# Kernel optimization log

Hardware: AMD Instinct MI355X
Metric: run time of the kernel (lower is better)

## Reference

```python
import jax, jax.numpy as jnp
import numpy as np

B, S, E = 4, 2048, 1024
H = 16
HD = E // H  # head_dim = 64


def setup_inputs() -> dict:
    key = jax.random.key(0)
    ks = jax.random.split(key, 12)
    sc = 0.02
    return {
        "q_encodings": jax.random.normal(ks[0], (B, S, E), jnp.float32),
        "k_encodings": jax.random.normal(ks[1], (B, S, E), jnp.float32),
        "v_encodings": jax.random.normal(ks[2], (B, S, E), jnp.float32),
        # per-head q/k/v linear weights [H, HD, HD] and biases [H, HD]
        "Wq": jax.random.normal(ks[3], (H, HD, HD), jnp.float32) * sc,
        "bq": jax.random.normal(ks[4], (H, HD), jnp.float32) * sc,
        "Wk": jax.random.normal(ks[5], (H, HD, HD), jnp.float32) * sc,
        "bk": jax.random.normal(ks[6], (H, HD), jnp.float32) * sc,
        "Wv": jax.random.normal(ks[7], (H, HD, HD), jnp.float32) * sc,
        "bv": jax.random.normal(ks[8], (H, HD), jnp.float32) * sc,
        # output projection [E, E] + bias [E]
        "Wp": jax.random.normal(ks[9], (E, E), jnp.float32) * sc,
        "bp": jax.random.normal(ks[10], (E,), jnp.float32) * sc,
        "mask": 1,
    }


def reference(q_encodings, k_encodings, v_encodings, Wq, bq, Wk, bk, Wv, bv, Wp, bp, mask):
    b, s, e = q_encodings.shape
    h, hd, _ = Wq.shape
    split = lambda x: x.reshape(b, s, h, hd)  # per-head slices of n_embd
    # batched per-head linear projections (original loops over heads)
    Q = jnp.einsum('bshd,hde->bshe', split(q_encodings), Wq) + bq
    K = jnp.einsum('bshd,hde->bshe', split(k_encodings), Wk) + bk
    V = jnp.einsum('bshd,hde->bshe', split(v_encodings), Wv) + bv
    # scaled dot-product scores [B,H,S,S]; scale uses head_dim (Attention.n_embd)
    scores = jnp.einsum('bqhd,bkhd->bhqk', Q, K) / jnp.sqrt(jnp.float32(hd))
    if mask:  # static Python flag, matches torch `if mask:`
        causal = jnp.tril(jnp.ones((s, s), jnp.float32))
        scores = scores + jnp.where(causal == 0, jnp.float32(-jnp.inf), jnp.float32(0.0))
    attn = jax.nn.softmax(scores, axis=-1)
    ctx = jnp.einsum('bhqk,bkhd->bqhd', attn, V).reshape(b, s, e)
    return ctx @ Wp + bp
```

## Files before the change

kernel.cpp:

```cpp
#include <hip/hip_runtime.h>
#include <hip/hip_bf16.h>
#include <math.h>

typedef __bf16 bf16;
typedef __bf16 bf16x8 __attribute__((ext_vector_type(8)));
typedef float f32x4 __attribute__((ext_vector_type(4)));
typedef unsigned int u32x2 __attribute__((ext_vector_type(2)));

constexpr int B = 4, S = 2048, E = 1024, H = 16, HD = 64;

constexpr float QSCALE = 0.125f * 1.44269504088896340736f;
constexpr float DTHR = 11.5f;

static __device__ __forceinline__ float exp2_fast(float x) {
#if __has_builtin(__builtin_amdgcn_exp2f)
    return __builtin_amdgcn_exp2f(x);
#else
    float r; asm("v_exp_f32 %0, %1" : "=v"(r) : "v"(x)); return r;
#endif
}

static __device__ __forceinline__ unsigned pk_bf16(float a, float b) {
    union { bf16 h[2]; unsigned u; } r;
    r.h[0] = (bf16)a; r.h[1] = (bf16)b;
    return r.u;
}

__global__ __launch_bounds__(256) void prep_weights(
    const float* __restrict__ Wq, const float* __restrict__ Wk,
    const float* __restrict__ Wv, const float* __restrict__ Wp,
    bf16* __restrict__ Wt, bf16* __restrict__ Wpt)
{
    __shared__ float t[64][65];
    const int tid = threadIdx.x;
    const int x = blockIdx.x, y = blockIdx.y;
    if (y < 3) {
        const int h = x, p = y;
        const float* W = (p == 0) ? Wq : (p == 1) ? Wk : Wv;
        const float scale = (p == 0) ? QSCALE : 1.0f;
        #pragma unroll
        for (int i = 0; i < 16; ++i) {
            int idx = tid + i * 256;
            int d = idx >> 6, e = idx & 63;
            t[d][e] = W[(size_t)h * 4096 + d * 64 + e];
        }
        __syncthreads();
        bf16* dst = Wt + ((size_t)p * H + h) * 4096;
        #pragma unroll
        for (int i = 0; i < 16; ++i) {
            int idx = tid + i * 256;
            int e = idx >> 6, d = idx & 63;
            dst[e * 64 + d] = (bf16)(t[d][e] * scale);
        }
    } else {
        const int k0 = (y - 3) * 64, n0 = x * 64;
        #pragma unroll
        for (int i = 0; i < 16; ++i) {
            int idx = tid + i * 256;
            int r = idx >> 6, c = idx & 63;
            t[r][c] = Wp[(size_t)(k0 + r) * E + n0 + c];
        }
        __syncthreads();
        #pragma unroll
        for (int i = 0; i < 16; ++i) {
            int idx = tid + i * 256;
            int r = idx >> 6, c = idx & 63;
            Wpt[(size_t)(n0 + r) * E + k0 + c] = (bf16)t[c][r];
        }
    }
}

__global__ __launch_bounds__(256) void qkv_proj(
    const float* __restrict__ xq, const float* __restrict__ xk, const float* __restrict__ xv,
    const bf16* __restrict__ Wt,
    const float* __restrict__ bq, const float* __restrict__ bk, const float* __restrict__ bv,
    bf16* __restrict__ Qb, bf16* __restrict__ Kb, bf16* __restrict__ Vt)
{
    const int b = blockIdx.z, h = blockIdx.y, s0 = blockIdx.x * 128;
    const int tid = threadIdx.x;
    const int w = tid >> 6, l = tid & 63;
    const int l16 = l & 15, lg = l >> 4;
    const size_t bh = (size_t)b * H + h;

    __shared__ __align__(16) bf16 xs[128][64];
    __shared__ __align__(16) bf16 Wl[64][64];
    __shared__ __align__(16) bf16 ts[10240];

    for (int p = 0; p < 3; ++p) {
        const float* x    = (p == 0) ? xq : (p == 1) ? xk : xv;
        const float* bias = (p == 0) ? bq : (p == 1) ? bk : bv;
        const float  bsc  = (p == 0) ? QSCALE : 1.0f;

        __syncthreads();
        #pragma unroll
        for (int i = 0; i < 4; ++i) {
            int idx = tid + i * 256;
            int r = idx >> 3, g = idx & 7;
            const float* src = &x[((size_t)b * S + s0 + r) * E + h * 64 + g * 8];
            float4 f0 = *(const float4*)src;
            float4 f1 = *(const float4*)(src + 4);
            union { bf16 h8[8]; uint4 u; } pk;
            pk.h8[0] = (bf16)f0.x; pk.h8[1] = (bf16)f0.y;
            pk.h8[2] = (bf16)f0.z; pk.h8[3] = (bf16)f0.w;
            pk.h8[4] = (bf16)f1.x; pk.h8[5] = (bf16)f1.y;
            pk.h8[6] = (bf16)f1.z; pk.h8[7] = (bf16)f1.w;
            *(uint4*)&xs[r][(g ^ (r & 7)) * 8] = pk.u;
        }
        const bf16* wsrc = Wt + ((size_t)p * H + h) * 4096;
        #pragma unroll
        for (int i = 0; i < 2; ++i) {
            int idx = tid + i * 256;
            int e = idx >> 3, g = idx & 7;
            *(uint4*)&Wl[e][(g ^ (e & 7)) * 8] = *(const uint4*)(wsrc + e * 64 + g * 8);
        }
        __syncthreads();

        if (p < 2) {
            float bcol[4];
            #pragma unroll
            for (int ei = 0; ei < 4; ++ei)
                bcol[ei] = bias[h * 64 + ei * 16 + l16] * bsc;
            #pragma unroll
            for (int st = 0; st < 2; ++st) {
                const int srow = w * 32 + st * 16 + l16;
                bf16x8 a0 = *(const bf16x8*)&xs[srow][((lg    ) ^ (srow & 7)) * 8];
                bf16x8 a1 = *(const bf16x8*)&xs[srow][((4 + lg) ^ (srow & 7)) * 8];
                #pragma unroll
                for (int ei = 0; ei < 4; ++ei) {
                    const int erow = ei * 16 + l16;
                    bf16x8 b0 = *(const bf16x8*)&Wl[erow][((lg    ) ^ (erow & 7)) * 8];
                    bf16x8 b1 = *(const bf16x8*)&Wl[erow][((4 + lg) ^ (erow & 7)) * 8];
                    f32x4 acc = {0.f, 0.f, 0.f, 0.f};
                    acc = __builtin_amdgcn_mfma_f32_16x16x32_bf16(a0, b0, acc, 0, 0, 0);
                    acc = __builtin_amdgcn_mfma_f32_16x16x32_bf16(a1, b1, acc, 0, 0, 0);
                    #pragma unroll
                    for (int r = 0; r < 4; ++r)
                        ts[(w * 32 + st * 16 + 4 * lg + r) * 80 + ei * 16 + l16] =
                            (bf16)(acc[r] + bcol[ei]);
                }
            }
            __syncthreads();
            bf16* out = (p == 0) ? Qb : Kb;
            #pragma unroll
            for (int i = 0; i < 4; ++i) {
                int idx = tid + i * 256;
                int r = idx >> 3, g = idx & 7;
                uint4 v = *(const uint4*)&ts[r * 80 + g * 8];
                *(uint4*)(out + (bh * S + s0 + r) * 64 + g * 8) = v;
            }
        } else {
            float brow[4];
            #pragma unroll
            for (int r = 0; r < 4; ++r)
                brow[r] = bias[h * 64 + w * 16 + 4 * lg + r];
            const int erow = w * 16 + l16;
            bf16x8 a0 = *(const bf16x8*)&Wl[erow][((lg    ) ^ (erow & 7)) * 8];
            bf16x8 a1 = *(const bf16x8*)&Wl[erow][((4 + lg) ^ (erow & 7)) * 8];
            #pragma unroll
            for (int st = 0; st < 8; ++st) {
                const int srow = st * 16 + l16;
                bf16x8 b0 = *(const bf16x8*)&xs[srow][((lg    ) ^ (srow & 7)) * 8];
                bf16x8 b1 = *(const bf16x8*)&xs[srow][((4 + lg) ^ (srow & 7)) * 8];
                f32x4 acc = {0.f, 0.f, 0.f, 0.f};
                acc = __builtin_amdgcn_mfma_f32_16x16x32_bf16(a0, b0, acc, 0, 0, 0);
                acc = __builtin_amdgcn_mfma_f32_16x16x32_bf16(a1, b1, acc, 0, 0, 0);
                #pragma unroll
                for (int r = 0; r < 4; ++r)
                    ts[(w * 16 + 4 * lg + r) * 136 + st * 16 + l16] =
                        (bf16)(acc[r] + brow[r]);
            }
            __syncthreads();
            #pragma unroll
            for (int i = 0; i < 4; ++i) {
                int idx = tid + i * 256;
                int r = idx >> 4, g = idx & 15;
                uint4 v = *(const uint4*)&ts[r * 136 + g * 8];
                *(uint4*)(Vt + (bh * 64 + r) * S + s0 + g * 8) = v;
            }
        }
    }
}

__global__ __launch_bounds__(512) void attn(
    const bf16* __restrict__ Qb, const bf16* __restrict__ Kb,
    const bf16* __restrict__ Vt, bf16* __restrict__ ctx)
{
    const int pair = blockIdx.x;
    const int bh   = blockIdx.y;
    const int b = bh >> 4, h = bh & 15;
    const int tid = threadIdx.x;
    const int w = tid >> 6;
    const int l = tid & 63;
    const int l16 = l & 15, lg = l >> 4;

    __shared__ __align__(16) bf16 Kl[2][64][64];
    __shared__ __align__(16) bf16 Vl[2][64][64];
    __shared__ __align__(16) bf16 Pl[8][16][72];

    const bf16* Qp = Qb + (size_t)bh * S * 64;
    const bf16* Kp = Kb + (size_t)bh * S * 64;
    const bf16* Vp = Vt + (size_t)bh * 64 * S;

    const int str = tid >> 3;
    const int stc = tid & 7;
    const int sws = (stc ^ (str & 7)) * 8;

    int foff0[4], foff1[4];
    #pragma unroll
    for (int s = 0; s < 4; ++s) {
        foff0[s] = (16 * s + l16) * 64 + ((lg    ) ^ (l16 & 7)) * 8;
        foff1[s] = (16 * s + l16) * 64 + ((4 + lg) ^ (l16 & 7)) * 8;
    }
    bf16* Plw = &Pl[w][0][0];
    const int pwr = l16 * 72 + 4 * lg;
    const int prd = l16 * 72 + 8 * lg;

    const bf16 one_ = (bf16)1.0f;
    const bf16x8 ones = {one_, one_, one_, one_, one_, one_, one_, one_};

    #pragma unroll 1
    for (int half = 0; half < 2; ++half) {
        const int qt   = half ? (15 - pair) : pair;
        const int qw0  = qt * 128 + w * 16;
        const int qabs = qw0 + l16;
        const int nt   = 2 * qt + 2;

        bf16x8 qf0 = *(const bf16x8*)(Qp + (size_t)qabs * 64 + lg * 8);
        bf16x8 qf1 = *(const bf16x8*)(Qp + (size_t)qabs * 64 + 32 + lg * 8);

        f32x4 o[4] = {};
        float m_run = -1e30f, l_run = 0.f;

        {
            uint4 kreg = *(const uint4*)(Kp + (size_t)str * 64 + stc * 8);
            uint4 vreg = *(const uint4*)(Vp + (size_t)str * S + stc * 8);
            *(uint4*)&Kl[0][str][sws] = kreg;
            *(uint4*)&Vl[0][str][sws] = vreg;
        }
        int cur = 0;
        for (int t = 0; t < nt; ++t) {
            __syncthreads();
            const bool pfv = (t + 1 < nt);
            uint4 kreg, vreg;
            if (pfv) {
                const int kv1 = (t + 1) * 64;
                kreg = *(const uint4*)(Kp + (size_t)(kv1 + str) * 64 + stc * 8);
                vreg = *(const uint4*)(Vp + (size_t)str * S + kv1 + stc * 8);
            }
            const int kv0 = t * 64;
            if (kv0 < qw0 + 16) {
                const bf16* Kbase = &Kl[cur][0][0];
                const bf16* Vbase = &Vl[cur][0][0];

                float p[16];
                __builtin_amdgcn_s_setprio(1);
                #pragma unroll
                for (int s = 0; s < 4; ++s) {
                    f32x4 sc = {0.f, 0.f, 0.f, 0.f};
                    bf16x8 ka = *(const bf16x8*)(Kbase + foff0[s]);
                    bf16x8 kb = *(const bf16x8*)(Kbase + foff1[s]);
                    sc = __builtin_amdgcn_mfma_f32_16x16x32_bf16(ka, qf0, sc, 0, 0, 0);
                    sc = __builtin_amdgcn_mfma_f32_16x16x32_bf16(kb, qf1, sc, 0, 0, 0);
                    p[4 * s + 0] = sc[0]; p[4 * s + 1] = sc[1];
                    p[4 * s + 2] = sc[2]; p[4 * s + 3] = sc[3];
                }
                __builtin_amdgcn_s_setprio(0);

                if (kv0 + 63 > qw0) {
                    #pragma unroll
                    for (int i = 0; i < 16; ++i) {
                        const int kvloc = 16 * (i >> 2) + 4 * lg + (i & 3);
                        if (kv0 + kvloc > qabs) p[i] = -1e30f;
                    }
                }

                float mx = p[0];
                #pragma unroll
                for (int i = 1; i < 16; ++i) mx = fmaxf(mx, p[i]);
                mx = fmaxf(mx, __shfl_xor(mx, 16));
                mx = fmaxf(mx, __shfl_xor(mx, 32));
                if (!__all(mx <= m_run + DTHR)) {
                    const float m_new = fmaxf(m_run, mx);
                    const float corr = exp2_fast(m_run - m_new);
                    l_run *= corr;
                    #pragma unroll
                    for (int ds = 0; ds < 4; ++ds) {
                        o[ds][0] *= corr; o[ds][1] *= corr;
                        o[ds][2] *= corr; o[ds][3] *= corr;
                    }
                    m_run = m_new;
                }
                #pragma unroll
                for (int i = 0; i < 16; ++i) p[i] = exp2_fast(p[i] - m_run);

                #pragma unroll
                for (int s = 0; s < 4; ++s) {
                    u32x2 pw;
                    pw[0] = pk_bf16(p[4 * s + 0], p[4 * s + 1]);
                    pw[1] = pk_bf16(p[4 * s + 2], p[4 * s + 3]);
                    *(u32x2*)(Plw + pwr + 16 * s) = pw;
                }
                asm volatile("s_waitcnt lgkmcnt(0)" ::: "memory");
                bf16x8 pf0 = *(const bf16x8*)(Plw + prd);
                bf16x8 pf1 = *(const bf16x8*)(Plw + prd + 32);

                __builtin_amdgcn_s_setprio(1);
                f32x4 o5 = {0.f, 0.f, 0.f, 0.f};
                o5 = __builtin_amdgcn_mfma_f32_16x16x32_bf16(ones, pf0, o5, 0, 0, 0);
                o5 = __builtin_amdgcn_mfma_f32_16x16x32_bf16(ones, pf1, o5, 0, 0, 0);
                #pragma unroll
                for (int ds = 0; ds < 4; ++ds) {
                    bf16x8 v0 = *(const bf16x8*)(Vbase + foff0[ds]);
                    bf16x8 v1 = *(const bf16x8*)(Vbase + foff1[ds]);
                    o[ds] = __builtin_amdgcn_mfma_f32_16x16x32_bf16(v0, pf0, o[ds], 0, 0, 0);
                    o[ds] = __builtin_amdgcn_mfma_f32_16x16x32_bf16(v1, pf1, o[ds], 0, 0, 0);
                }
                __builtin_amdgcn_s_setprio(0);
                l_run += o5[0];
            }
            if (pfv) {
                *(uint4*)&Kl[cur ^ 1][str][sws] = kreg;
                *(uint4*)&Vl[cur ^ 1][str][sws] = vreg;
            }
            cur ^= 1;
        }

        const float il = 1.0f / l_run;
        bf16* crow = ctx + ((size_t)b * S + qabs) * E + h * 64;
        #pragma unroll
        for (int ds = 0; ds < 4; ++ds) {
            u32x2 pw;
            pw[0] = pk_bf16(o[ds][0] * il, o[ds][1] * il);
            pw[1] = pk_bf16(o[ds][2] * il, o[ds][3] * il);
            *(u32x2*)(crow + 16 * ds + 4 * lg) = pw;
        }
    }
}

__global__ __launch_bounds__(256) void out_gemm(
    const bf16* __restrict__ A, const bf16* __restrict__ Bt,
    const float* __restrict__ bp, float* __restrict__ C)
{
    const int n0 = blockIdx.x * 128, m0 = blockIdx.y * 128;
    const int tid = threadIdx.x;
    const int w = tid >> 6, l = tid & 63;
    const int l16 = l & 15, lg = l >> 4;
    const int wm = w >> 1, wn = w & 1;

    __shared__ __align__(16) bf16 Al[128][64];
    __shared__ __align__(16) bf16 Bl[128][64];

    f32x4 acc[4][4] = {};

    for (int k0 = 0; k0 < E; k0 += 64) {
        __syncthreads();
        #pragma unroll
        for (int i = 0; i < 4; ++i) {
            int row = (tid >> 3) + i * 32;
            int c = tid & 7;
            int cs = c ^ (row & 7);
            *(uint4*)&Al[row][cs * 8] =
                *(const uint4*)(A + (size_t)(m0 + row) * E + k0 + c * 8);
            *(uint4*)&Bl[row][cs * 8] =
                *(const uint4*)(Bt + (size_t)(n0 + row) * E + k0 + c * 8);
        }
        __syncthreads();

        #pragma unroll
        for (int ks = 0; ks < 2; ++ks) {
            bf16x8 af[4], bfr[4];
            #pragma unroll
            for (int mi = 0; mi < 4; ++mi) {
                int r = wm * 64 + mi * 16 + l16;
                af[mi] = *(const bf16x8*)&Al[r][((ks * 4 + lg) ^ (r & 7)) * 8];
            }
            #pragma unroll
            for (int ni = 0; ni < 4; ++ni) {
                int r = wn * 64 + ni * 16 + l16;
                bfr[ni] = *(const bf16x8*)&Bl[r][((ks * 4 + lg) ^ (r & 7)) * 8];
            }
            #pragma unroll
            for (int mi = 0; mi < 4; ++mi)
                #pragma unroll
                for (int ni = 0; ni < 4; ++ni)
                    acc[mi][ni] = __builtin_amdgcn_mfma_f32_16x16x32_bf16(
                        af[mi], bfr[ni], acc[mi][ni], 0, 0, 0);
        }
    }

    #pragma unroll
    for (int ni = 0; ni < 4; ++ni) {
        const int col = n0 + wn * 64 + ni * 16 + l16;
        const float bias = bp[col];
        #pragma unroll
        for (int mi = 0; mi < 4; ++mi) {
            #pragma unroll
            for (int e = 0; e < 4; ++e) {
                int row = m0 + wm * 64 + mi * 16 + 4 * lg + e;
                C[(size_t)row * E + col] = acc[mi][ni][e] + bias;
            }
        }
    }
}

extern "C" void kernel_launch(void* const* d_in, const int* in_sizes, int n_in,
                              void* d_out, int out_size, void* d_ws, size_t ws_size,
                              hipStream_t stream)
{
    const float* xq = (const float*)d_in[0];
    const float* xk = (const float*)d_in[1];
    const float* xv = (const float*)d_in[2];
    const float* Wq = (const float*)d_in[3];
    const float* bq = (const float*)d_in[4];
    const float* Wk = (const float*)d_in[5];
    const float* bk = (const float*)d_in[6];
    const float* Wv = (const float*)d_in[7];
    const float* bv = (const float*)d_in[8];
    const float* Wp = (const float*)d_in[9];
    const float* bp = (const float*)d_in[10];
    float* out = (float*)d_out;

    char* ws = (char*)d_ws;
    const size_t sz_bhse = (size_t)B * H * S * HD;
    bf16* Qb  = (bf16*)ws;  ws += sz_bhse * 2;
    bf16* Kb  = (bf16*)ws;  ws += sz_bhse * 2;
    bf16* Vtw = (bf16*)ws;  ws += sz_bhse * 2;
    bf16* ctx = (bf16*)ws;  ws += (size_t)B * S * E * 2;
    bf16* Wpt = (bf16*)ws;  ws += (size_t)E * E * 2;
    bf16* Wt3 = (bf16*)ws;  ws += (size_t)3 * H * HD * HD * 2;

    prep_weights<<<dim3(16, 19), 256, 0, stream>>>(Wq, Wk, Wv, Wp, Wt3, Wpt);
    qkv_proj<<<dim3(S / 128, H, B), 256, 0, stream>>>(xq, xk, xv, Wt3,
                                                      bq, bk, bv, Qb, Kb, Vtw);
    attn<<<dim3(8, B * H), 512, 0, stream>>>(Qb, Kb, Vtw, ctx);
    out_gemm<<<dim3(E / 128, (B * S) / 128), 256, 0, stream>>>(ctx, Wpt, bp, out);
}
```

Measured before the change: 123.2 us.

## Stage K/V and GEMM tiles with direct global-to-LDS loads

Both the causal attention kernel and the output-projection GEMM now copy their K/V and A/B tiles straight from global memory into LDS with `global_load_lds`, instead of loading into registers and writing them back with `ds_write`. The XOR swizzle moves from the LDS destination to the per-lane source chunk, so each wave's 1 KB write lands linearly while the read layout stays the same. This removes the register staging and LDS store instructions and frees VGPRs. In exchange, correctness now depends on the barrier waiting for the outstanding DMA loads. The row max in the softmax is also rebuilt as a tree reduction to shorten the dependency chain.

```diff
diff --git a/kernel.cpp b/kernel.cpp
--- a/kernel.cpp
+++ b/kernel.cpp
@@ -24,6 +24,13 @@
     union { bf16 h[2]; unsigned u; } r;
     r.h[0] = (bf16)a; r.h[1] = (bf16)b;
     return r.u;
+}
+
+static __device__ __forceinline__ void gl16(const void* g, void* l) {
+    __builtin_amdgcn_global_load_lds(
+        (__attribute__((address_space(1))) void*)g,
+        (__attribute__((address_space(3))) void*)l,
+        16, 0, 0);
 }
 
 __global__ __launch_bounds__(256) void prep_weights(
@@ -201,9 +208,13 @@
     const bf16* Kp = Kb + (size_t)bh * S * 64;
     const bf16* Vp = Vt + (size_t)bh * 64 * S;
 
-    const int str = tid >> 3;
-    const int stc = tid & 7;
-    const int sws = (stc ^ (str & 7)) * 8;
+    const int r8 = l >> 3;
+    const int kr = 8 * w + r8;
+    const int chunk = ((l & 7) ^ r8) * 8;
+    const bf16* ksrc = Kp + (size_t)kr * 64 + chunk;
+    const bf16* vsrc = Vp + (size_t)kr * S + chunk;
+    bf16* const klds = &Kl[0][8 * w][0];
+    bf16* const vlds = &Vl[0][8 * w][0];
 
     int foff0[4], foff1[4];
     #pragma unroll
@@ -231,21 +242,15 @@
         f32x4 o[4] = {};
         float m_run = -1e30f, l_run = 0.f;
 
-        {
-            uint4 kreg = *(const uint4*)(Kp + (size_t)str * 64 + stc * 8);
-            uint4 vreg = *(const uint4*)(Vp + (size_t)str * S + stc * 8);
-            *(uint4*)&Kl[0][str][sws] = kreg;
-            *(uint4*)&Vl[0][str][sws] = vreg;
-        }
+        gl16(ksrc, klds);
+        gl16(vsrc, vlds);
+
         int cur = 0;
         for (int t = 0; t < nt; ++t) {
             __syncthreads();
-            const bool pfv = (t + 1 < nt);
-            uint4 kreg, vreg;
-            if (pfv) {
-                const int kv1 = (t + 1) * 64;
-                kreg = *(const uint4*)(Kp + (size_t)(kv1 + str) * 64 + stc * 8);
-                vreg = *(const uint4*)(Vp + (size_t)str * S + kv1 + stc * 8);
+            if (t + 1 < nt) {
+                gl16(ksrc + (size_t)(t + 1) * 4096, klds + (cur ^ 1) * 4096);
+                gl16(vsrc + (size_t)(t + 1) * 64,   vlds + (cur ^ 1) * 4096);
             }
             const int kv0 = t * 64;
             if (kv0 < qw0 + 16) {
@@ -274,9 +279,11 @@
                     }
                 }
 
-                float mx = p[0];
-                #pragma unroll
-                for (int i = 1; i < 16; ++i) mx = fmaxf(mx, p[i]);
+                float m4[4];
+                #pragma unroll
+                for (int j = 0; j < 4; ++j)
+                    m4[j] = fmaxf(fmaxf(p[4*j], p[4*j+1]), fmaxf(p[4*j+2], p[4*j+3]));
+                float mx = fmaxf(fmaxf(m4[0], m4[1]), fmaxf(m4[2], m4[3]));
                 mx = fmaxf(mx, __shfl_xor(mx, 16));
                 mx = fmaxf(mx, __shfl_xor(mx, 32));
                 if (!__all(mx <= m_run + DTHR)) {
@@ -318,10 +325,6 @@
                 __builtin_amdgcn_s_setprio(0);
                 l_run += o5[0];
             }
-            if (pfv) {
-                *(uint4*)&Kl[cur ^ 1][str][sws] = kreg;
-                *(uint4*)&Vl[cur ^ 1][str][sws] = vreg;
-            }
             cur ^= 1;
         }
 
@@ -352,17 +355,16 @@
 
     f32x4 acc[4][4] = {};
 
+    const int r8 = l >> 3;
+    const int chunk = ((l & 7) ^ r8) * 8;
+
     for (int k0 = 0; k0 < E; k0 += 64) {
         __syncthreads();
         #pragma unroll
         for (int i = 0; i < 4; ++i) {
-            int row = (tid >> 3) + i * 32;
-            int c = tid & 7;
-            int cs = c ^ (row & 7);
-            *(uint4*)&Al[row][cs * 8] =
-                *(const uint4*)(A + (size_t)(m0 + row) * E + k0 + c * 8);
-            *(uint4*)&Bl[row][cs * 8] =
-                *(const uint4*)(Bt + (size_t)(n0 + row) * E + k0 + c * 8);
+            const int rb = 8 * w + 32 * i;
+            gl16(A  + (size_t)(m0 + rb + r8) * E + k0 + chunk, &Al[rb][0]);
+            gl16(Bt + (size_t)(n0 + rb + r8) * E + k0 + chunk, &Bl[rb][0]);
         }
         __syncthreads();
 
```

New measurement: 125.0 us. Within noise of the previous version (+1.5%).
